# Kernel optimization log

Measured on AMD Instinct MI355X. Metric: run time of the kernel, lower is better.

The kernel has to match this reference:

```python
import jax, jax.numpy as jnp
import numpy as np

TEMPERATURE = 0.07


def setup_inputs() -> dict:
    key = jax.random.key(0)
    embeddings = jax.random.normal(key, (16384, 256), dtype=jnp.float32)
    return {"embeddings": embeddings}


def reference(embeddings) -> jnp.ndarray:
    # L2 normalize rows (torch F.normalize uses eps clamp 1e-12)
    norm = jnp.maximum(jnp.linalg.norm(embeddings, axis=1, keepdims=True), 1e-12)
    emb = embeddings / norm
    # [N, N] similarity, temperature-scaled logits
    logits = jnp.matmul(emb, emb.T) / TEMPERATURE
    # cross entropy against diagonal labels (labels[i] = i)
    logp = jax.nn.log_softmax(logits, axis=1)
    loss = -jnp.mean(jnp.diagonal(logp))
    return loss
```

## Files before the change

kernel.cpp:

```cpp
#include <hip/hip_runtime.h>
#include <hip/hip_bf16.h>

typedef __bf16 bf16;
typedef __attribute__((ext_vector_type(8))) __bf16 bf16x8;
typedef __attribute__((ext_vector_type(4))) __bf16 bf16x4;
typedef __attribute__((ext_vector_type(16))) float f32x16;

#define N_ROWS 16384
#define DIM 256
#define NT 128
#define NJC 256
#define LSTRIP 8
#define NSTRIPS 2112
#define SQK1 4.53981608f
#define LN2F 0.69314718056f

#define WS_T_OFF (N_ROWS * DIM * 2)
#define WS_D_OFF (WS_T_OFF + N_ROWS * 4)

#define GLOAD_LDS(g, l)                                        \
    __builtin_amdgcn_global_load_lds(                          \
        (const __attribute__((address_space(1))) void*)(g),    \
        (__attribute__((address_space(3))) void*)(l), 16, 0, 0)

__global__ void __launch_bounds__(256) normalize_kernel(const float* __restrict__ in,
                                                        bf16* __restrict__ out,
                                                        float* __restrict__ Tg,
                                                        float* __restrict__ Dg,
                                                        float* __restrict__ loss_out) {
    if (blockIdx.x == 0 && threadIdx.x == 0) loss_out[0] = 0.0f;
    if (blockIdx.x < 64) Tg[blockIdx.x * 256 + threadIdx.x] = 0.0f;

    const int row  = blockIdx.x * 4 + (threadIdx.x >> 6);
    const int lane = threadIdx.x & 63;
    const float4* rp = (const float4*)(in + (size_t)row * DIM);
    float4 v = rp[lane];
    float ss = v.x * v.x + v.y * v.y + v.z * v.z + v.w * v.w;
#pragma unroll
    for (int m = 1; m < 64; m <<= 1) ss += __shfl_xor(ss, m, 64);
    float inv = SQK1 / fmaxf(sqrtf(ss), 1e-12f);
    bf16x4 o;
    o[0] = (bf16)(v.x * inv);
    o[1] = (bf16)(v.y * inv);
    o[2] = (bf16)(v.z * inv);
    o[3] = (bf16)(v.w * inv);
    *(bf16x4*)(out + (size_t)row * DIM + lane * 4) = o;

    float f0 = (float)o[0], f1 = (float)o[1], f2 = (float)o[2], f3 = (float)o[3];
    float s2 = f0 * f0 + f1 * f1 + f2 * f2 + f3 * f3;
#pragma unroll
    for (int m = 1; m < 64; m <<= 1) s2 += __shfl_xor(s2, m, 64);
    if (lane == 0) Dg[row] = s2;
}

#define TREE16(R, out)                                                     \
    do {                                                                   \
        float w8[8], w4[4], w2[2], w1, g_;                                 \
        _Pragma("unroll") for (int i_ = 0; i_ < 8; ++i_) {                 \
            g_ = (lo & 16) ? R[i_] : R[i_ + 8];                            \
            w8[i_] = ((lo & 16) ? R[i_ + 8] : R[i_]) + __shfl_xor(g_, 16); \
        }                                                                  \
        _Pragma("unroll") for (int i_ = 0; i_ < 4; ++i_) {                 \
            g_ = (lo & 8) ? w8[i_] : w8[i_ + 4];                           \
            w4[i_] = ((lo & 8) ? w8[i_ + 4] : w8[i_]) + __shfl_xor(g_, 8); \
        }                                                                  \
        _Pragma("unroll") for (int i_ = 0; i_ < 2; ++i_) {                 \
            g_ = (lo & 4) ? w4[i_] : w4[i_ + 2];                           \
            w2[i_] = ((lo & 4) ? w4[i_ + 2] : w4[i_]) + __shfl_xor(g_, 4); \
        }                                                                  \
        g_ = (lo & 2) ? w2[0] : w2[1];                                     \
        w1 = ((lo & 2) ? w2[1] : w2[0]) + __shfl_xor(g_, 2);               \
        out = w1 + __shfl_xor(w1, 1);                                      \
    } while (0)

__global__ void __launch_bounds__(256, 2)
loss_kernel(const bf16* __restrict__ A, float* __restrict__ Tg) {
    __shared__ bf16 Bs0[64 * DIM];
    __shared__ bf16 Bs1[64 * DIM];
    __shared__ float CsAcc[2][LSTRIP][64];

    const int tid = threadIdx.x;
    const int w  = tid >> 6;
    const int l  = tid & 63;
    const int lo = l & 31, hi = l >> 5;
    const int rg = w >> 1;
    const int cg = w & 1;

    int it = 0, rem = blockIdx.x;
    for (;;) {
        int nch = (NJC - 2 * it + LSTRIP - 1) >> 3;
        if (rem < nch) break;
        rem -= nch;
        ++it;
    }
    const int jc0 = 2 * it + rem * LSTRIP;
    const int jc1 = (jc0 + LSTRIP < NJC) ? (jc0 + LSTRIP) : NJC;

    const int arow = rg * 64;

    bf16x8 af0[16], af1[16];
    {
        const bf16* ap0 = A + (size_t)(it * 128 + arow + lo) * DIM + hi * 8;
#pragma unroll
        for (int k = 0; k < 16; ++k) {
            af0[k] = *(const volatile bf16x8*)(ap0 + k * 16);
            af1[k] = *(const volatile bf16x8*)(ap0 + 32 * DIM + k * 16);
        }
    }

    float s0[16], s1[16];
#pragma unroll
    for (int r = 0; r < 16; ++r) { s0[r] = 0.f; s1[r] = 0.f; }

    const int s_dma = l & 31;
    const int rl    = l >> 5;
    int vo[4];
#pragma unroll
    for (int j = 0; j < 4; ++j) {
        const int c = (s_dma & 24) | ((s_dma & 7) ^ ((j * 2 + rl) & 7));
        vo[j] = rl * DIM + c * 8;
    }

    const int rbase = (cg * 32 + lo) * DIM;
    const int mx7 = lo & 7;

#define ISSUE(jcn, BUF)                                                      \
    do {                                                                     \
        const bf16* tb_ = A + (size_t)((jcn) * 64 + w * 16) * DIM;           \
        bf16* lb_ = &BUF[(w * 16) * DIM];                                    \
        _Pragma("unroll") for (int q_ = 0; q_ < 8; ++q_) {                   \
            GLOAD_LDS(tb_ + (q_ * 2) * DIM + vo[q_ & 3],                     \
                      lb_ + (q_ * 2) * DIM);                                 \
        }                                                                    \
    } while (0)

#define TILE_BODY(BR, BW, jc, t)                                             \
    do {                                                                     \
        asm volatile("s_barrier" ::: "memory");                              \
        if ((jc) + 1 < jc1) {                                                \
            ISSUE((jc) + 1, BW);                                             \
            asm volatile("s_waitcnt vmcnt(8)" ::: "memory");                 \
        } else {                                                             \
            asm volatile("s_waitcnt vmcnt(0)" ::: "memory");                 \
        }                                                                    \
        asm volatile("s_barrier" ::: "memory");                              \
        f32x16 c0, c1;                                                       \
        _Pragma("unroll") for (int r_ = 0; r_ < 16; ++r_) {                  \
            c0[r_] = 0.f; c1[r_] = 0.f;                                      \
        }                                                                    \
        _Pragma("unroll") for (int k_ = 0; k_ < 16; ++k_) {                  \
            const int cc_ = k_ * 2 + hi;                                     \
            const int slot_ = (cc_ & 24) | ((cc_ & 7) ^ mx7);                \
            bf16x8 b_ = *(const bf16x8*)&BR[rbase + slot_ * 8];              \
            c0 = __builtin_amdgcn_mfma_f32_32x32x16_bf16(af0[k_], b_, c0, 0, 0, 0); \
            c1 = __builtin_amdgcn_mfma_f32_32x32x16_bf16(af1[k_], b_, c1, 0, 0, 0); \
        }                                                                    \
        float cs_ = 0.f;                                                     \
        _Pragma("unroll") for (int r_ = 0; r_ < 16; ++r_) {                  \
            float e0_ = __builtin_amdgcn_exp2f(c0[r_]);                      \
            float e1_ = __builtin_amdgcn_exp2f(c1[r_]);                      \
            s0[r_] += e0_;                                                   \
            s1[r_] += e1_;                                                   \
            cs_ += e0_ + e1_;                                                \
        }                                                                    \
        cs_ += __shfl_xor(cs_, 32);                                          \
        if (hi == 0) CsAcc[rg][t][cg * 32 + lo] = cs_;                       \
    } while (0)

    ISSUE(jc0, Bs0);
    int jc = jc0;
    while (jc < jc1) {
        TILE_BODY(Bs0, Bs1, jc, jc - jc0);
        ++jc;
        if (jc >= jc1) break;
        TILE_BODY(Bs1, Bs0, jc, jc - jc0);
        ++jc;
    }

    float t0, t1;
    TREE16(s0, t0);
    TREE16(s1, t1);
    const int r = (lo >> 1) & 15;
    const int rowoff = (r & 3) + 8 * (r >> 2) + 4 * hi;
    atomicAdd(&Tg[it * 128 + arow + ((l & 1) ? 32 : 0) + rowoff], (l & 1) ? t1 : t0);

    __syncthreads();
    const int nt_strip = jc1 - jc0;
    for (int i = tid; i < nt_strip * 64; i += 256) {
        const int t = i >> 6, col = i & 63;
        if (((jc0 + t) >> 1) != it) {
            atomicAdd(&Tg[(jc0 + t) * 64 + col],
                      CsAcc[0][t][col] + CsAcc[1][t][col]);
        }
    }
#undef ISSUE
#undef TILE_BODY
}

__global__ void __launch_bounds__(256) final_kernel(const float* __restrict__ Tg,
                                                    const float* __restrict__ Dg,
                                                    float* __restrict__ out) {
    __shared__ float red[4];
    const int i = blockIdx.x * 256 + threadIdx.x;
    float c = LN2F * (__log2f(Tg[i]) - Dg[i]) * (1.0f / (float)N_ROWS);
#pragma unroll
    for (int m = 1; m < 64; m <<= 1) c += __shfl_xor(c, m, 64);
    if ((threadIdx.x & 63) == 0) red[threadIdx.x >> 6] = c;
    __syncthreads();
    if (threadIdx.x == 0)
        atomicAdd(out, red[0] + red[1] + red[2] + red[3]);
}

extern "C" void kernel_launch(void* const* d_in, const int* in_sizes, int n_in,
                              void* d_out, int out_size, void* d_ws, size_t ws_size,
                              hipStream_t stream) {
    const float* emb = (const float*)d_in[0];
    float* out = (float*)d_out;
    bf16* Abf = (bf16*)d_ws;
    float* Tg = (float*)((char*)d_ws + WS_T_OFF);
    float* Dg = (float*)((char*)d_ws + WS_D_OFF);

    hipLaunchKernelGGL(normalize_kernel, dim3(N_ROWS / 4), dim3(256), 0, stream,
                       emb, Abf, Tg, Dg, out);
    hipLaunchKernelGGL(loss_kernel, dim3(NSTRIPS), dim3(256), 0, stream,
                       Abf, Tg);
    hipLaunchKernelGGL(final_kernel, dim3(N_ROWS / 256), dim3(256), 0, stream,
                       Tg, Dg, out);
}
```

Baseline: 174.0 us.

## Split 128-row A block across 8 waves with one MFMA accumulator each

New measurement: 167.7 us. 3.6% less time.

```diff
diff --git a/kernel.cpp b/kernel.cpp
--- a/kernel.cpp
+++ b/kernel.cpp
@@ -73,11 +73,11 @@
         out = w1 + __shfl_xor(w1, 1);                                      \
     } while (0)
 
-__global__ void __launch_bounds__(256, 2)
+__global__ void __launch_bounds__(512, 4)
 loss_kernel(const bf16* __restrict__ A, float* __restrict__ Tg) {
     __shared__ bf16 Bs0[64 * DIM];
     __shared__ bf16 Bs1[64 * DIM];
-    __shared__ float CsAcc[2][LSTRIP][64];
+    __shared__ float CsAcc[4][LSTRIP][64];
 
     const int tid = threadIdx.x;
     const int w  = tid >> 6;
@@ -96,29 +96,25 @@
     const int jc0 = 2 * it + rem * LSTRIP;
     const int jc1 = (jc0 + LSTRIP < NJC) ? (jc0 + LSTRIP) : NJC;
 
-    const int arow = rg * 64;
-
-    bf16x8 af0[16], af1[16];
+    bf16x8 af[16];
     {
-        const bf16* ap0 = A + (size_t)(it * 128 + arow + lo) * DIM + hi * 8;
-#pragma unroll
-        for (int k = 0; k < 16; ++k) {
-            af0[k] = *(const volatile bf16x8*)(ap0 + k * 16);
-            af1[k] = *(const volatile bf16x8*)(ap0 + 32 * DIM + k * 16);
-        }
-    }
-
-    float s0[16], s1[16];
-#pragma unroll
-    for (int r = 0; r < 16; ++r) { s0[r] = 0.f; s1[r] = 0.f; }
+        const bf16* ap = A + (size_t)(it * 128 + rg * 32 + lo) * DIM + hi * 8;
+#pragma unroll
+        for (int k = 0; k < 16; ++k)
+            af[k] = *(const volatile bf16x8*)(ap + k * 16);
+    }
+
+    float s0[16];
+#pragma unroll
+    for (int r = 0; r < 16; ++r) s0[r] = 0.f;
 
     const int s_dma = l & 31;
     const int rl    = l >> 5;
     int vo[4];
 #pragma unroll
-    for (int j = 0; j < 4; ++j) {
-        const int c = (s_dma & 24) | ((s_dma & 7) ^ ((j * 2 + rl) & 7));
-        vo[j] = rl * DIM + c * 8;
+    for (int q = 0; q < 4; ++q) {
+        const int c = (s_dma & 24) | ((s_dma & 7) ^ ((q * 2 + rl) & 7));
+        vo[q] = rl * DIM + c * 8;
     }
 
     const int rbase = (cg * 32 + lo) * DIM;
@@ -126,10 +122,10 @@
 
 #define ISSUE(jcn, BUF)                                                      \
     do {                                                                     \
-        const bf16* tb_ = A + (size_t)((jcn) * 64 + w * 16) * DIM;           \
-        bf16* lb_ = &BUF[(w * 16) * DIM];                                    \
-        _Pragma("unroll") for (int q_ = 0; q_ < 8; ++q_) {                   \
-            GLOAD_LDS(tb_ + (q_ * 2) * DIM + vo[q_ & 3],                     \
+        const bf16* tb_ = A + (size_t)((jcn) * 64 + w * 8) * DIM;            \
+        bf16* lb_ = &BUF[(w * 8) * DIM];                                     \
+        _Pragma("unroll") for (int q_ = 0; q_ < 4; ++q_) {                   \
+            GLOAD_LDS(tb_ + (q_ * 2) * DIM + vo[q_],                         \
                       lb_ + (q_ * 2) * DIM);                                 \
         }                                                                    \
     } while (0)
@@ -139,29 +135,24 @@
         asm volatile("s_barrier" ::: "memory");                              \
         if ((jc) + 1 < jc1) {                                                \
             ISSUE((jc) + 1, BW);                                             \
-            asm volatile("s_waitcnt vmcnt(8)" ::: "memory");                 \
+            asm volatile("s_waitcnt vmcnt(4)" ::: "memory");                 \
         } else {                                                             \
             asm volatile("s_waitcnt vmcnt(0)" ::: "memory");                 \
         }                                                                    \
         asm volatile("s_barrier" ::: "memory");                              \
-        f32x16 c0, c1;                                                       \
-        _Pragma("unroll") for (int r_ = 0; r_ < 16; ++r_) {                  \
-            c0[r_] = 0.f; c1[r_] = 0.f;                                      \
-        }                                                                    \
+        f32x16 c0;                                                           \
+        _Pragma("unroll") for (int r_ = 0; r_ < 16; ++r_) c0[r_] = 0.f;      \
         _Pragma("unroll") for (int k_ = 0; k_ < 16; ++k_) {                  \
             const int cc_ = k_ * 2 + hi;                                     \
             const int slot_ = (cc_ & 24) | ((cc_ & 7) ^ mx7);                \
             bf16x8 b_ = *(const bf16x8*)&BR[rbase + slot_ * 8];              \
-            c0 = __builtin_amdgcn_mfma_f32_32x32x16_bf16(af0[k_], b_, c0, 0, 0, 0); \
-            c1 = __builtin_amdgcn_mfma_f32_32x32x16_bf16(af1[k_], b_, c1, 0, 0, 0); \
+            c0 = __builtin_amdgcn_mfma_f32_32x32x16_bf16(af[k_], b_, c0, 0, 0, 0); \
         }                                                                    \
         float cs_ = 0.f;                                                     \
         _Pragma("unroll") for (int r_ = 0; r_ < 16; ++r_) {                  \
-            float e0_ = __builtin_amdgcn_exp2f(c0[r_]);                      \
-            float e1_ = __builtin_amdgcn_exp2f(c1[r_]);                      \
-            s0[r_] += e0_;                                                   \
-            s1[r_] += e1_;                                                   \
-            cs_ += e0_ + e1_;                                                \
+            float e_ = __builtin_amdgcn_exp2f(c0[r_]);                       \
+            s0[r_] += e_;                                                    \
+            cs_ += e_;                                                       \
         }                                                                    \
         cs_ += __shfl_xor(cs_, 32);                                          \
         if (hi == 0) CsAcc[rg][t][cg * 32 + lo] = cs_;                       \
@@ -177,20 +168,21 @@
         ++jc;
     }
 
-    float t0, t1;
+    float t0;
     TREE16(s0, t0);
-    TREE16(s1, t1);
     const int r = (lo >> 1) & 15;
     const int rowoff = (r & 3) + 8 * (r >> 2) + 4 * hi;
-    atomicAdd(&Tg[it * 128 + arow + ((l & 1) ? 32 : 0) + rowoff], (l & 1) ? t1 : t0);
+    if ((l & 1) == 0)
+        atomicAdd(&Tg[it * 128 + rg * 32 + rowoff], t0);
 
     __syncthreads();
     const int nt_strip = jc1 - jc0;
-    for (int i = tid; i < nt_strip * 64; i += 256) {
+    for (int i = tid; i < nt_strip * 64; i += 512) {
         const int t = i >> 6, col = i & 63;
         if (((jc0 + t) >> 1) != it) {
             atomicAdd(&Tg[(jc0 + t) * 64 + col],
-                      CsAcc[0][t][col] + CsAcc[1][t][col]);
+                      CsAcc[0][t][col] + CsAcc[1][t][col] +
+                      CsAcc[2][t][col] + CsAcc[3][t][col]);
         }
     }
 #undef ISSUE
@@ -222,7 +214,7 @@
 
     hipLaunchKernelGGL(normalize_kernel, dim3(N_ROWS / 4), dim3(256), 0, stream,
                        emb, Abf, Tg, Dg, out);
-    hipLaunchKernelGGL(loss_kernel, dim3(NSTRIPS), dim3(256), 0, stream,
+    hipLaunchKernelGGL(loss_kernel, dim3(NSTRIPS), dim3(512), 0, stream,
                        Abf, Tg);
     hipLaunchKernelGGL(final_kernel, dim3(N_ROWS / 256), dim3(256), 0, stream,
                        Tg, Dg, out);
```
